# Performance work log

Hardware: AMD Instinct MI355X
Metric: run time of the kernel (lower is better)

## Reference

```python
import jax, jax.numpy as jnp
import numpy as np

N_NODES = 40000
N_EDGES = 640000
N_GRAPHS = 64
D = 128


def setup_inputs() -> dict:
    key = jax.random.key(0)
    ks = jax.random.split(key, 8)
    x = jax.random.normal(ks[0], (N_NODES, D), dtype=jnp.float32)
    edge_index = jax.random.randint(ks[1], (2, N_EDGES), 0, N_NODES, dtype=jnp.int64)
    batch = jnp.sort(jax.random.randint(ks[2], (N_NODES,), 0, N_GRAPHS, dtype=jnp.int64))
    s = 1.0 / np.sqrt(D)
    W_rel1 = jax.random.normal(ks[3], (D, D), dtype=jnp.float32) * s
    W_root1 = jax.random.normal(ks[4], (D, D), dtype=jnp.float32) * s
    W_rel2 = jax.random.normal(ks[5], (D, D), dtype=jnp.float32) * s
    W_root2 = jax.random.normal(ks[6], (D, D), dtype=jnp.float32) * s
    Wc = jax.random.normal(ks[7], (D, D), dtype=jnp.float32) * s
    b1 = jnp.zeros((D,), jnp.float32)
    b2 = jnp.zeros((D,), jnp.float32)
    bc = jnp.zeros((D,), jnp.float32)
    return dict(x=x, edge_index=edge_index, batch=batch,
                W_rel1=W_rel1, W_root1=W_root1, b1=b1,
                W_rel2=W_rel2, W_root2=W_root2, b2=b2,
                Wc=Wc, bc=bc)


def _graph_conv(x, src, dst, W_rel, W_root, b):
    # PyG GraphConv with mean aggregation:
    # out_i = W_rel @ mean_{j in N(i)} x_j + W_root @ x_i + b
    n = x.shape[0]
    msg = x[src]                                              # [E, D] gather
    agg = jax.ops.segment_sum(msg, dst, num_segments=n)       # [N, D]
    deg = jax.ops.segment_sum(jnp.ones_like(dst, dtype=x.dtype), dst, num_segments=n)
    agg = agg / jnp.maximum(deg, 1.0)[:, None]                # mean, 0 if isolated
    return agg @ W_rel.T + x @ W_root.T + b


def reference(x, edge_index, batch, W_rel1, W_root1, b1, W_rel2, W_root2, b2, Wc, bc):
    src, dst = edge_index[0], edge_index[1]
    h = jax.nn.relu(_graph_conv(x, src, dst, W_rel1, W_root1, b1))
    h = jax.nn.relu(_graph_conv(h, src, dst, W_rel2, W_root2, b2))
    # global_mean_pool (dropout is identity in eval mode)
    sums = jax.ops.segment_sum(h, batch, num_segments=N_GRAPHS)          # [G, D]
    cnts = jax.ops.segment_sum(jnp.ones_like(batch, dtype=h.dtype), batch, num_segments=N_GRAPHS)
    pooled = sums / jnp.maximum(cnts, 1.0)[:, None]
    return pooled @ Wc.T + bc
```

## Files before the change

### kernel.cpp

```cpp
#include <hip/hip_runtime.h>

#define DD 128
#define ANODE 4
#define REC 64
#define MAXD 62

typedef __attribute__((ext_vector_type(8))) short short8v;
typedef __attribute__((ext_vector_type(4))) float float4v;

static __device__ __forceinline__ unsigned short f2bf(float f) {
  unsigned int u = __float_as_uint(f);
  u = (u + 0x7fffu + ((u >> 16) & 1u)) >> 16;
  return (unsigned short)u;
}
static __device__ __forceinline__ float bf2f(unsigned short h) {
  return __uint_as_float(((unsigned int)h) << 16);
}
static __device__ __forceinline__ float blo(unsigned int u) {
  return __uint_as_float(u << 16);
}
static __device__ __forceinline__ float bhi(unsigned int u) {
  return __uint_as_float(u & 0xffff0000u);
}
static __device__ __forceinline__ unsigned int pk(float lo, float hi) {
  return (unsigned int)f2bf(lo) | ((unsigned int)f2bf(hi) << 16);
}

__global__ void prep_kernel(unsigned short* __restrict__ recs, float* __restrict__ sums,
                            int N, int nsums,
                            const float* __restrict__ Wr1, const float* __restrict__ Wo1,
                            const float* __restrict__ Wr2, const float* __restrict__ Wo2,
                            unsigned short* __restrict__ Bpk) {
  int i = blockIdx.x * blockDim.x + threadIdx.x;
  if (i < N) *reinterpret_cast<int*>(recs + (size_t)i * REC) = 0;
  if (i < nsums) sums[i] = 0.f;
  if (i < 8192) {
    int L = i >> 12, rest = i & 4095;
    int kt = rest >> 9, nt = (rest >> 6) & 7, lane = rest & 63;
    int d = nt * 16 + (lane & 15);
    int kbase = kt * 32 + (lane >> 4) * 8;
    const float* Wrel = L ? Wr2 : Wr1;
    const float* Wroot = L ? Wo2 : Wo1;
    unsigned short* o = Bpk + (size_t)i * 8;
    #pragma unroll
    for (int j = 0; j < 8; ++j) {
      int k = kbase + j;
      float w = (k < DD) ? Wrel[d * DD + k] : Wroot[d * DD + (k - DD)];
      o[j] = f2bf(w);
    }
  }
}

__global__ void build_kernel(const int* __restrict__ src, const int* __restrict__ dst,
                             unsigned short* __restrict__ recs, int E, int eb,
                             const float* __restrict__ x, unsigned short* __restrict__ XH,
                             unsigned short* __restrict__ XL, int N, int has_lo) {
  int b = blockIdx.x;
  if (b < eb) {
    int e = b * 256 + threadIdx.x;
    if (e < E) {
      int d = dst[e];
      unsigned short* rec = recs + (size_t)d * REC;
      int p = atomicAdd(reinterpret_cast<int*>(rec), 1);
      if (p < MAXD) rec[2 + p] = (unsigned short)src[e];
    }
  } else {
    int i = (b - eb) * 256 + threadIdx.x;
    if (i < N * 32) {
      float4 v = reinterpret_cast<const float4*>(x)[i];
      ushort4 h;
      h.x = f2bf(v.x); h.y = f2bf(v.y); h.z = f2bf(v.z); h.w = f2bf(v.w);
      reinterpret_cast<ushort4*>(XH)[i] = h;
      if (has_lo) {
        ushort4 l;
        l.x = f2bf(v.x - bf2f(h.x)); l.y = f2bf(v.y - bf2f(h.y));
        l.z = f2bf(v.z - bf2f(h.z)); l.w = f2bf(v.w - bf2f(h.w));
        reinterpret_cast<ushort4*>(XL)[i] = l;
      }
    }
  }
}

__global__ __launch_bounds__(256) void gather3(
    const uint4* __restrict__ X4, const unsigned short* __restrict__ recs,
    uint4* __restrict__ AH4, int N) {
  int node = blockIdx.x * ANODE + (threadIdx.x >> 6);
  if (node >= N) return;
  int lane = threadIdx.x & 63;
  int sub = lane >> 4;
  int sl = lane & 15;
  const unsigned short* rec = recs + (size_t)node * REC;
  int dg = *reinterpret_cast<const int*>(rec);
  if (dg > MAXD) dg = MAXD;
  const unsigned short* csr = rec + 2;
  int pe = dg;
  float a0 = 0.f, a1 = 0.f, a2 = 0.f, a3 = 0.f, a4 = 0.f, a5 = 0.f, a6 = 0.f, a7 = 0.f;
  int p = 0;
  for (; p + 8 <= pe; p += 8) {
    int s0 = csr[p + sub];
    int s1 = csr[p + 4 + sub];
    uint4 u0 = X4[(size_t)s0 * 16 + sl];
    uint4 u1 = X4[(size_t)s1 * 16 + sl];
    a0 += blo(u0.x) + blo(u1.x);  a1 += bhi(u0.x) + bhi(u1.x);
    a2 += blo(u0.y) + blo(u1.y);  a3 += bhi(u0.y) + bhi(u1.y);
    a4 += blo(u0.z) + blo(u1.z);  a5 += bhi(u0.z) + bhi(u1.z);
    a6 += blo(u0.w) + blo(u1.w);  a7 += bhi(u0.w) + bhi(u1.w);
  }
  for (; p < pe; p += 4) {
    int q = p + sub;
    bool act = q < pe;
    int s0 = act ? (int)csr[q] : 0;
    uint4 u0 = X4[(size_t)s0 * 16 + sl];
    if (act) {
      a0 += blo(u0.x); a1 += bhi(u0.x);
      a2 += blo(u0.y); a3 += bhi(u0.y);
      a4 += blo(u0.z); a5 += bhi(u0.z);
      a6 += blo(u0.w); a7 += bhi(u0.w);
    }
  }
  #define RED2(v) v += __shfl_xor(v, 16, 64); v += __shfl_xor(v, 32, 64);
  RED2(a0) RED2(a1) RED2(a2) RED2(a3) RED2(a4) RED2(a5) RED2(a6) RED2(a7)
  #undef RED2
  float inv = 1.f / fmaxf((float)dg, 1.f);
  a0 *= inv; a1 *= inv; a2 *= inv; a3 *= inv;
  a4 *= inv; a5 *= inv; a6 *= inv; a7 *= inv;
  if (sub == 0) {
    uint4 h;
    h.x = pk(a0, a1); h.y = pk(a2, a3); h.z = pk(a4, a5); h.w = pk(a6, a7);
    AH4[(size_t)node * 16 + sl] = h;
  }
}

__global__ __launch_bounds__(256) void gemm2(
    const unsigned short* __restrict__ AH,
    const unsigned short* __restrict__ XH, const unsigned short* __restrict__ XL,
    const unsigned short* __restrict__ Bpk, const float* __restrict__ bias,
    unsigned short* __restrict__ HH, unsigned short* __restrict__ HL,
    float* __restrict__ sums, const int* __restrict__ batch,
    int N, int has_lo) {
  int lane = threadIdx.x & 63;
  int wid = threadIdx.x >> 6;
  int m0 = (blockIdx.x * 4 + wid) * 16;
  if (m0 >= N) return;
  int arow = m0 + (lane & 15);
  if (arow >= N) arow = N - 1;
  int koff = (lane >> 4) * 8;
  const short8v* Bf = (const short8v*)Bpk;
  float4v acc[8];
  #pragma unroll
  for (int nt = 0; nt < 8; ++nt) acc[nt] = (float4v){0.f, 0.f, 0.f, 0.f};

  #pragma unroll
  for (int kt = 0; kt < 8; ++kt) {
    if (kt < 4) {
      short8v a = *reinterpret_cast<const short8v*>(AH + (size_t)arow * DD + kt * 32 + koff);
      #pragma unroll
      for (int nt = 0; nt < 8; ++nt) {
        short8v b = Bf[(kt * 8 + nt) * 64 + lane];
        acc[nt] = __builtin_amdgcn_mfma_f32_16x16x32_bf16(a, b, acc[nt], 0, 0, 0);
      }
    } else {
      int o = (kt - 4) * 32 + koff;
      short8v xh = *reinterpret_cast<const short8v*>(XH + (size_t)arow * DD + o);
      if (has_lo) {
        short8v xl = *reinterpret_cast<const short8v*>(XL + (size_t)arow * DD + o);
        #pragma unroll
        for (int nt = 0; nt < 8; ++nt) {
          short8v b = Bf[(kt * 8 + nt) * 64 + lane];
          acc[nt] = __builtin_amdgcn_mfma_f32_16x16x32_bf16(xh, b, acc[nt], 0, 0, 0);
          acc[nt] = __builtin_amdgcn_mfma_f32_16x16x32_bf16(xl, b, acc[nt], 0, 0, 0);
        }
      } else {
        #pragma unroll
        for (int nt = 0; nt < 8; ++nt) {
          short8v b = Bf[(kt * 8 + nt) * 64 + lane];
          acc[nt] = __builtin_amdgcn_mfma_f32_16x16x32_bf16(xh, b, acc[nt], 0, 0, 0);
        }
      }
    }
  }

  int col0 = lane & 15;
  int rbase = m0 + (lane >> 4) * 4;
  if (sums) {
    int gl = batch[m0];
    int me = (m0 + 15 < N) ? m0 + 15 : N - 1;
    int gh = batch[me];
    bool fast = (gl == gh) && (m0 + 16 <= N);
    #pragma unroll
    for (int nt = 0; nt < 8; ++nt) {
      int col = nt * 16 + col0;
      float bv = bias[col];
      float v0 = fmaxf(acc[nt][0] + bv, 0.f);
      float v1 = fmaxf(acc[nt][1] + bv, 0.f);
      float v2 = fmaxf(acc[nt][2] + bv, 0.f);
      float v3 = fmaxf(acc[nt][3] + bv, 0.f);
      if (fast) {
        float s = (v0 + v1) + (v2 + v3);
        s += __shfl_xor(s, 16, 64);
        s += __shfl_xor(s, 32, 64);
        if (lane < 16) atomicAdd(&sums[gl * DD + col], s);
      } else {
        float vv[4] = {v0, v1, v2, v3};
        #pragma unroll
        for (int r = 0; r < 4; ++r) {
          int row = rbase + r;
          if (row < N) atomicAdd(&sums[batch[row] * DD + col], vv[r]);
        }
      }
    }
  } else {
    #pragma unroll
    for (int nt = 0; nt < 8; ++nt) {
      int col = nt * 16 + col0;
      float bv = bias[col];
      #pragma unroll
      for (int r = 0; r < 4; ++r) {
        int row = rbase + r;
        if (row < N) {
          float v = fmaxf(acc[nt][r] + bv, 0.f);
          unsigned short h = f2bf(v);
          HH[(size_t)row * DD + col] = h;
          if (has_lo) HL[(size_t)row * DD + col] = f2bf(v - bf2f(h));
        }
      }
    }
  }
}

__global__ void final_kernel(const float* __restrict__ sums, const int* __restrict__ batch,
                             const float* __restrict__ Wc, const float* __restrict__ bc,
                             float* __restrict__ out, int N, int G) {
  int g = blockIdx.x;
  int d = threadIdx.x;
  __shared__ float p[DD];
  __shared__ float invs;
  if (d == 0) {
    int lo = 0, hi = N;
    while (lo < hi) { int m = (lo + hi) >> 1; if (batch[m] < g) lo = m + 1; else hi = m; }
    int a = lo;
    lo = 0; hi = N;
    while (lo < hi) { int m = (lo + hi) >> 1; if (batch[m] < g + 1) lo = m + 1; else hi = m; }
    invs = 1.0f / fmaxf((float)(lo - a), 1.0f);
  }
  __syncthreads();
  p[d] = sums[g * DD + d] * invs;
  __syncthreads();
  float acc = bc[d];
  #pragma unroll 8
  for (int k = 0; k < DD; ++k) acc += p[k] * Wc[d * DD + k];
  out[g * DD + d] = acc;
}

extern "C" void kernel_launch(void* const* d_in, const int* in_sizes, int n_in,
                              void* d_out, int out_size, void* d_ws, size_t ws_size,
                              hipStream_t stream) {
  const float* x   = (const float*)d_in[0];
  const int*   ei  = (const int*)d_in[1];
  const int* batch = (const int*)d_in[2];
  const float* Wr1 = (const float*)d_in[3];
  const float* Wo1 = (const float*)d_in[4];
  const float* b1  = (const float*)d_in[5];
  const float* Wr2 = (const float*)d_in[6];
  const float* Wo2 = (const float*)d_in[7];
  const float* b2  = (const float*)d_in[8];
  const float* Wc  = (const float*)d_in[9];
  const float* bc  = (const float*)d_in[10];
  float* out = (float*)d_out;

  const int N = in_sizes[0] / DD;
  const int E = in_sizes[1] / 2;
  const int G = out_size / DD;
  const int* src = ei;
  const int* dst = ei + E;

  unsigned short* recs = (unsigned short*)d_ws;
  float* sums = (float*)(recs + (size_t)N * REC);
  unsigned short* Bpk = (unsigned short*)(sums + (size_t)G * DD);

  unsigned short* actbase = Bpk + 65536;
  size_t fixed = (size_t)((char*)actbase - (char*)d_ws);
  size_t arr = (size_t)N * DD * sizeof(unsigned short);
  int has_lo = (ws_size >= fixed + 5 * arr) ? 1 : 0;

  unsigned short* XH = actbase;
  unsigned short* HH = XH + (size_t)N * DD;
  unsigned short* AH = HH + (size_t)N * DD;
  unsigned short* XL = has_lo ? AH + (size_t)N * DD : nullptr;
  unsigned short* HL = has_lo ? XL + (size_t)N * DD : nullptr;

  const int blk = 256;
  int prep_n = (N * 32 > 8192) ? N : N;
  int prep_threads = N;
  if (G * DD > prep_threads) prep_threads = G * DD;
  if (8192 > prep_threads) prep_threads = 8192;
  prep_kernel<<<(prep_threads + blk - 1) / blk, blk, 0, stream>>>(
      recs, sums, N, G * DD, Wr1, Wo1, Wr2, Wo2, Bpk);
  (void)prep_n;

  int eb = (E + blk - 1) / blk;
  int xb = (N * 32 + blk - 1) / blk;
  build_kernel<<<eb + xb, blk, 0, stream>>>(src, dst, recs, E, eb, x, XH, XL, N, has_lo);

  int agg_blocks = (N + ANODE - 1) / ANODE;
  int gemm_blocks = (N + 63) / 64;

  gather3<<<agg_blocks, 256, 0, stream>>>((const uint4*)XH, recs, (uint4*)AH, N);
  gemm2<<<gemm_blocks, 256, 0, stream>>>(AH, XH, XL, Bpk, b1,
                                         HH, HL, nullptr, nullptr, N, has_lo);
  gather3<<<agg_blocks, 256, 0, stream>>>((const uint4*)HH, recs, (uint4*)AH, N);
  gemm2<<<gemm_blocks, 256, 0, stream>>>(AH, HH, HL, Bpk + 32768, b2,
                                         nullptr, nullptr, sums, batch, N, has_lo);

  final_kernel<<<G, DD, 0, stream>>>(sums, batch, Wc, bc, out, N, G);
}
```

Baseline: 150.6 us.

## Privatize edge-bucketing counters across eight copies and stage GEMM weights in LDS

Edge insertion now spreads atomics over eight private per-node counter/slot arrays, chosen by block index, to reduce contention on a single per-node counter. A new merge kernel then compacts them into the existing per-node record. The GEMM kernel also copies the packed weight fragments into shared memory once per block instead of reading them from global memory in the inner loop. The cost is an extra kernel launch, a larger workspace, and 64KB of LDS per GEMM block, which may lower occupancy.

```diff
diff --git a/kernel.cpp b/kernel.cpp
--- a/kernel.cpp
+++ b/kernel.cpp
@@ -4,6 +4,8 @@
 #define ANODE 4
 #define REC 64
 #define MAXD 62
+#define CSLOT 24
+#define NC 8
 
 typedef __attribute__((ext_vector_type(8))) short short8v;
 typedef __attribute__((ext_vector_type(4))) float float4v;
@@ -26,13 +28,15 @@
   return (unsigned int)f2bf(lo) | ((unsigned int)f2bf(hi) << 16);
 }
 
-__global__ void prep_kernel(unsigned short* __restrict__ recs, float* __restrict__ sums,
-                            int N, int nsums,
+__global__ void prep_kernel(int* __restrict__ cnt8, int ncnt8,
+                            unsigned short* __restrict__ recs, int nhdr,
+                            float* __restrict__ sums, int nsums,
                             const float* __restrict__ Wr1, const float* __restrict__ Wo1,
                             const float* __restrict__ Wr2, const float* __restrict__ Wo2,
                             unsigned short* __restrict__ Bpk) {
   int i = blockIdx.x * blockDim.x + threadIdx.x;
-  if (i < N) *reinterpret_cast<int*>(recs + (size_t)i * REC) = 0;
+  if (i < ncnt8) cnt8[i] = 0;
+  if (i < nhdr) *reinterpret_cast<int*>(recs + (size_t)i * REC) = 0;
   if (i < nsums) sums[i] = 0.f;
   if (i < 8192) {
     int L = i >> 12, rest = i & 4095;
@@ -51,10 +55,48 @@
   }
 }
 
-__global__ void build_kernel(const int* __restrict__ src, const int* __restrict__ dst,
-                             unsigned short* __restrict__ recs, int E, int eb,
-                             const float* __restrict__ x, unsigned short* __restrict__ XH,
-                             unsigned short* __restrict__ XL, int N, int has_lo) {
+static __device__ __forceinline__ void xsplit_body(int i, const float* __restrict__ x,
+                                                   unsigned short* __restrict__ XH,
+                                                   unsigned short* __restrict__ XL,
+                                                   int N, int has_lo) {
+  if (i < N * 32) {
+    float4 v = reinterpret_cast<const float4*>(x)[i];
+    ushort4 h;
+    h.x = f2bf(v.x); h.y = f2bf(v.y); h.z = f2bf(v.z); h.w = f2bf(v.w);
+    reinterpret_cast<ushort4*>(XH)[i] = h;
+    if (has_lo) {
+      ushort4 l;
+      l.x = f2bf(v.x - bf2f(h.x)); l.y = f2bf(v.y - bf2f(h.y));
+      l.z = f2bf(v.z - bf2f(h.z)); l.w = f2bf(v.w - bf2f(h.w));
+      reinterpret_cast<ushort4*>(XL)[i] = l;
+    }
+  }
+}
+
+__global__ void build8_kernel(const int* __restrict__ src, const int* __restrict__ dst,
+                              int* __restrict__ cnt8, unsigned short* __restrict__ slots8,
+                              int E, int eb,
+                              const float* __restrict__ x, unsigned short* __restrict__ XH,
+                              unsigned short* __restrict__ XL, int N, int has_lo) {
+  int b = blockIdx.x;
+  if (b < eb) {
+    int e = b * 256 + threadIdx.x;
+    if (e < E) {
+      int c = b & (NC - 1);
+      int d = dst[e];
+      int idx = c * N + d;
+      int p = atomicAdd(&cnt8[idx], 1);
+      if (p < CSLOT) slots8[(size_t)idx * CSLOT + p] = (unsigned short)src[e];
+    }
+  } else {
+    xsplit_body((b - eb) * 256 + threadIdx.x, x, XH, XL, N, has_lo);
+  }
+}
+
+__global__ void build1_kernel(const int* __restrict__ src, const int* __restrict__ dst,
+                              unsigned short* __restrict__ recs, int E, int eb,
+                              const float* __restrict__ x, unsigned short* __restrict__ XH,
+                              unsigned short* __restrict__ XL, int N, int has_lo) {
   int b = blockIdx.x;
   if (b < eb) {
     int e = b * 256 + threadIdx.x;
@@ -65,20 +107,30 @@
       if (p < MAXD) rec[2 + p] = (unsigned short)src[e];
     }
   } else {
-    int i = (b - eb) * 256 + threadIdx.x;
-    if (i < N * 32) {
-      float4 v = reinterpret_cast<const float4*>(x)[i];
-      ushort4 h;
-      h.x = f2bf(v.x); h.y = f2bf(v.y); h.z = f2bf(v.z); h.w = f2bf(v.w);
-      reinterpret_cast<ushort4*>(XH)[i] = h;
-      if (has_lo) {
-        ushort4 l;
-        l.x = f2bf(v.x - bf2f(h.x)); l.y = f2bf(v.y - bf2f(h.y));
-        l.z = f2bf(v.z - bf2f(h.z)); l.w = f2bf(v.w - bf2f(h.w));
-        reinterpret_cast<ushort4*>(XL)[i] = l;
-      }
-    }
-  }
+    xsplit_body((b - eb) * 256 + threadIdx.x, x, XH, XL, N, has_lo);
+  }
+}
+
+__global__ __launch_bounds__(256) void merge_kernel(const int* __restrict__ cnt8,
+                                                    const unsigned short* __restrict__ slots8,
+                                                    unsigned short* __restrict__ recs, int N) {
+  int wv = (blockIdx.x * 256 + threadIdx.x) >> 6;
+  int lane = threadIdx.x & 63;
+  if (wv >= N) return;
+  unsigned short* rec = recs + (size_t)wv * REC;
+  int total = 0;
+  #pragma unroll
+  for (int c = 0; c < NC; ++c) {
+    int k = cnt8[c * N + wv];
+    if (k > CSLOT) k = CSLOT;
+    if (lane < k) {
+      int pos = total + lane;
+      if (pos < MAXD) rec[2 + pos] = slots8[(size_t)(c * N + wv) * CSLOT + lane];
+    }
+    total += k;
+  }
+  if (total > MAXD) total = MAXD;
+  if (lane == 0) *reinterpret_cast<int*>(rec) = total;
 }
 
 __global__ __launch_bounds__(256) void gather3(
@@ -138,6 +190,15 @@
     unsigned short* __restrict__ HH, unsigned short* __restrict__ HL,
     float* __restrict__ sums, const int* __restrict__ batch,
     int N, int has_lo) {
+  __shared__ __align__(16) unsigned short Bl[32768];
+  {
+    const uint4* srcB = (const uint4*)Bpk;
+    uint4* dstB = (uint4*)Bl;
+    #pragma unroll
+    for (int i = threadIdx.x; i < 4096; i += 256) dstB[i] = srcB[i];
+  }
+  __syncthreads();
+
   int lane = threadIdx.x & 63;
   int wid = threadIdx.x >> 6;
   int m0 = (blockIdx.x * 4 + wid) * 16;
@@ -145,7 +206,7 @@
   int arow = m0 + (lane & 15);
   if (arow >= N) arow = N - 1;
   int koff = (lane >> 4) * 8;
-  const short8v* Bf = (const short8v*)Bpk;
+  const short8v* Bf = (const short8v*)Bl;
   float4v acc[8];
   #pragma unroll
   for (int nt = 0; nt < 8; ++nt) acc[nt] = (float4v){0.f, 0.f, 0.f, 0.f};
@@ -289,18 +350,31 @@
   unsigned short* XL = has_lo ? AH + (size_t)N * DD : nullptr;
   unsigned short* HL = has_lo ? XL + (size_t)N * DD : nullptr;
 
+  unsigned short* tail = has_lo ? HL + (size_t)N * DD : AH + (size_t)N * DD;
+  size_t priv_bytes = (size_t)NC * N * sizeof(int) + (size_t)NC * N * CSLOT * sizeof(unsigned short);
+  size_t used = (size_t)((char*)tail - (char*)d_ws);
+  int nc8 = (ws_size >= used + priv_bytes) ? 1 : 0;
+  int* cnt8 = nc8 ? (int*)tail : nullptr;
+  unsigned short* slots8 = nc8 ? (unsigned short*)(cnt8 + (size_t)NC * N) : nullptr;
+
   const int blk = 256;
-  int prep_n = (N * 32 > 8192) ? N : N;
-  int prep_threads = N;
+  int prep_threads = nc8 ? NC * N : N;
   if (G * DD > prep_threads) prep_threads = G * DD;
   if (8192 > prep_threads) prep_threads = 8192;
   prep_kernel<<<(prep_threads + blk - 1) / blk, blk, 0, stream>>>(
-      recs, sums, N, G * DD, Wr1, Wo1, Wr2, Wo2, Bpk);
-  (void)prep_n;
+      cnt8, nc8 ? NC * N : 0, recs, nc8 ? 0 : N, sums, G * DD,
+      Wr1, Wo1, Wr2, Wo2, Bpk);
 
   int eb = (E + blk - 1) / blk;
   int xb = (N * 32 + blk - 1) / blk;
-  build_kernel<<<eb + xb, blk, 0, stream>>>(src, dst, recs, E, eb, x, XH, XL, N, has_lo);
+  if (nc8) {
+    build8_kernel<<<eb + xb, blk, 0, stream>>>(src, dst, cnt8, slots8, E, eb,
+                                               x, XH, XL, N, has_lo);
+    merge_kernel<<<(N * 64 + blk - 1) / blk, blk, 0, stream>>>(cnt8, slots8, recs, N);
+  } else {
+    build1_kernel<<<eb + xb, blk, 0, stream>>>(src, dst, recs, E, eb,
+                                               x, XH, XL, N, has_lo);
+  }
 
   int agg_blocks = (N + ANODE - 1) / ANODE;
   int gemm_blocks = (N + 63) / 64;
```

Measured after the change: 184.6 us. 22.6% more time.
